# Performance work log

Hardware: AMD Instinct MI355X
Metric: run time of the kernel (lower is better)

Reference implementation:

```python
import jax, jax.numpy as jnp
import numpy as np

H, W, C = 24, 8, 128
HW = H * W  # 192
EPS = 1e-5


def setup_inputs() -> dict:
    key = jax.random.key(0)
    k1, k2 = jax.random.split(key)
    P, G = 64, 64
    prob_fea = jax.random.normal(k1, (P, C, H, W), dtype=jnp.float32)
    gal_fea = jax.random.normal(k2, (G, C, H, W), dtype=jnp.float32)
    bn_gamma = jnp.ones((1,), jnp.float32)
    bn_beta = jnp.zeros((1,), jnp.float32)
    # reset_parameters: fc.weight filled with 1/(H*W)
    fc_w = jnp.full((1, 2 * HW), 1.0 / HW, dtype=jnp.float32)
    fc_b = jnp.zeros((1,), jnp.float32)
    lbn_gamma = jnp.ones((1,), jnp.float32)
    lbn_beta = jnp.zeros((1,), jnp.float32)
    return {"prob_fea": prob_fea, "gal_fea": gal_fea, "bn_gamma": bn_gamma,
            "bn_beta": bn_beta, "fc_w": fc_w, "fc_b": fc_b,
            "lbn_gamma": lbn_gamma, "lbn_beta": lbn_beta}


def reference(prob_fea, gal_fea, bn_gamma, bn_beta, fc_w, fc_b, lbn_gamma, lbn_beta):
    P = prob_fea.shape[0]
    G = gal_fea.shape[0]
    pf = prob_fea.reshape(P, C, HW)  # [P, C, hw]
    gf = gal_fea.reshape(G, C, HW)   # [G, C, hw]
    # all-pairs spatial correlation: score[p, g, r, s] = sum_c pf[p,c,s] * gf[g,c,r]
    score = jnp.einsum('pcs,gcr->pgrs', pf, gf)  # [P, G, hw, hw]
    max_r = jnp.max(score, axis=2)  # max over gallery positions r -> [P, G, hw]
    max_s = jnp.max(score, axis=3)  # max over probe positions s   -> [P, G, hw]
    feat = jnp.concatenate((max_r, max_s), axis=-1).reshape(-1, 2 * HW)  # [P*G, 2hw]
    # BatchNorm1d(1) on [N, 1, 2hw] in training mode: stats over all N*2hw elems
    mu = jnp.mean(feat)
    var = jnp.var(feat)
    feat = (feat - mu) * jax.lax.rsqrt(var + EPS) * bn_gamma[0] + bn_beta[0]
    # fc: [P*G, 2hw] @ [2hw, 1] + b
    logit = feat @ fc_w.T + fc_b  # [P*G, 1]
    # BatchNorm1d(1) on [N, 1]: stats over N
    lmu = jnp.mean(logit)
    lvar = jnp.var(logit)
    logit = (logit - lmu) * jax.lax.rsqrt(lvar + EPS) * lbn_gamma[0] + lbn_beta[0]
    return logit.reshape(P, G)
```

## Files before the change

### kernel.cpp

```cpp
#include <hip/hip_runtime.h>
#include <hip/hip_bf16.h>
#include <stdint.h>

#define HW 192
#define NC 128
#define KEPS 1e-5f
#define QTB 12288

typedef __attribute__((ext_vector_type(8))) short short8;
typedef __attribute__((ext_vector_type(4))) float f32x4;

__device__ __forceinline__ float max3f(float a, float b, float c) {
  float d;
  asm("v_max3_f32 %0, %1, %2, %3" : "=v"(d) : "v"(a), "v"(b), "v"(c));
  return d;
}

__global__ __launch_bounds__(256)
void prep_kernel(const float* __restrict__ prob,
                 const float* __restrict__ gal,
                 unsigned short* __restrict__ probT,
                 unsigned short* __restrict__ galT) {
  __shared__ unsigned short lds[32 * 194];
  const int b = blockIdx.x;
  const int slice = b >> 2;
  const int cc = (b & 3) * 32;
  const bool isProbe = (slice < 64);
  const float* src = isProbe ? prob + (size_t)slice * NC * HW
                             : gal + (size_t)(slice - 64) * NC * HW;
  unsigned short* dst = isProbe ? probT + (size_t)slice * HW * NC
                                : galT + (size_t)(slice - 64) * HW * NC;
  const float* s0 = src + (size_t)cc * HW;
  #pragma unroll
  for (int k = 0; k < 24; ++k) {
    int i = k * 256 + threadIdx.x;
    int cp = i / HW;
    int hw = i - cp * HW;
    lds[cp * 194 + hw] =
        __builtin_bit_cast(unsigned short, __float2bfloat16(s0[i]));
  }
  __syncthreads();
  const int cp = threadIdx.x & 31;
  const int hw0 = threadIdx.x >> 5;
  const int c = cc + cp;
  #pragma unroll
  for (int k = 0; k < 24; ++k) {
    int hw = hw0 + 8 * k;
    unsigned short v = lds[cp * 194 + hw];
    int col = isProbe ? ((((2 * c) ^ ((hw & 7) << 4))) >> 1) : c;
    dst[hw * NC + col] = v;
  }
}

__device__ __forceinline__ void gl_lds16(const void* gsrc, void* ldst) {
  __builtin_amdgcn_global_load_lds(
      (const __attribute__((address_space(1))) void*)gsrc,
      (__attribute__((address_space(3))) void*)ldst, 16, 0, 0);
}

template <int CTRL>
__device__ __forceinline__ float dpp_max(float x) {
  int xi = __builtin_bit_cast(int, x);
  int yi = __builtin_amdgcn_update_dpp(xi, xi, CTRL, 0xf, 0xf, false);
  return fmaxf(x, __builtin_bit_cast(float, yi));
}
__device__ __forceinline__ float ror16_max(float x) {
  x = dpp_max<0x121>(x);
  x = dpp_max<0x122>(x);
  x = dpp_max<0x124>(x);
  x = dpp_max<0x128>(x);
  return x;
}

__global__ __launch_bounds__(256, 3)
void pair_kernel(const unsigned short* __restrict__ galT,
                 const unsigned short* __restrict__ probT,
                 const float* __restrict__ fc_w,
                 float* __restrict__ Wout,
                 float* __restrict__ sPart,
                 float* __restrict__ qPart) {
  __shared__ char ldsP[2][QTB];
  __shared__ float cmP[4][4][192];
  __shared__ float rmF[4][192];
  __shared__ float red[16];
  __shared__ float red2[8];

  const int tid = threadIdx.x;
  const int lane = tid & 63;
  const int wid = tid >> 6;
  const int q = lane >> 4;
  const int r16 = lane & 15;
  const int swz = (r16 & 7) << 4;

  const int g = blockIdx.x >> 4;
  const int pc = blockIdx.x & 15;

  const char* gbase = (const char*)(galT + (size_t)g * HW * NC);
  short8 a[3][4];
  #pragma unroll
  for (int m = 0; m < 3; ++m)
    #pragma unroll
    for (int ks = 0; ks < 4; ++ks)
      a[m][ks] = *(const short8*)(gbase + (wid * 48 + m * 16 + r16) * 256 + ks * 64 + q * 16);

  const float w0 = fc_w[tid];
  const float w1 = (tid < 128) ? fc_w[256 + tid] : 0.f;

  const char* pT = (const char*)probT + (size_t)(pc * 4) * 49152;

  #pragma unroll
  for (int ch = 0; ch < 3; ++ch)
    gl_lds16(pT + ch * 4096 + wid * 1024 + lane * 16,
             &ldsP[0][ch * 4096 + wid * 1024]);

  float rm[3][4];
  const f32x4 zz = (f32x4){0.f, 0.f, 0.f, 0.f};

  for (int t = 0; t < 16; ++t) {
    const int qc = t & 3;
    const int pi = t >> 2;
    __syncthreads();

    if (t + 1 < 16) {
      const char* src = pT + (size_t)(t + 1) * QTB;
      char* dst = ldsP[(t + 1) & 1];
      #pragma unroll
      for (int ch = 0; ch < 3; ++ch)
        gl_lds16(src + ch * 4096 + wid * 1024 + lane * 16,
                 dst + ch * 4096 + wid * 1024);
    }
    const char* cur = ldsP[t & 1];

    __builtin_amdgcn_s_setprio(1);
    f32x4 acc[3][3];
    #pragma unroll
    for (int n = 0; n < 3; ++n) {
      const char* rowB = cur + (n * 16 + r16) * 256;
      #pragma unroll
      for (int ks = 0; ks < 4; ++ks) {
        short8 bf = *(const short8*)(rowB + ((ks * 64 + q * 16) ^ swz));
        #pragma unroll
        for (int m = 0; m < 3; ++m)
          acc[m][n] = __builtin_amdgcn_mfma_f32_16x16x32_bf16(
              a[m][ks], bf, (ks == 0) ? zz : acc[m][n], 0, 0, 0);
      }
    }
    __builtin_amdgcn_s_setprio(0);

    #pragma unroll
    for (int n = 0; n < 3; ++n) {
      float m0 = max3f(acc[0][n][0], acc[0][n][1], acc[0][n][2]);
      float m1 = max3f(acc[0][n][3], acc[1][n][0], acc[1][n][1]);
      float m2 = max3f(acc[1][n][2], acc[1][n][3], acc[2][n][0]);
      float m3 = max3f(acc[2][n][1], acc[2][n][2], acc[2][n][3]);
      float cm = max3f(m0, m1, m2);
      cm = fmaxf(cm, m3);
      cm = fmaxf(cm, __shfl_xor(cm, 16));
      cm = fmaxf(cm, __shfl_xor(cm, 32));
      if (lane < 16) cmP[pi][wid][qc * 48 + n * 16 + r16] = cm;
    }
    #pragma unroll
    for (int m = 0; m < 3; ++m)
      #pragma unroll
      for (int j = 0; j < 4; ++j) {
        float v = max3f(acc[m][0][j], acc[m][1][j], acc[m][2][j]);
        rm[m][j] = (qc == 0) ? v : fmaxf(rm[m][j], v);
      }
    if (qc == 3) {
      #pragma unroll
      for (int m = 0; m < 3; ++m)
        #pragma unroll
        for (int j = 0; j < 4; ++j) {
          float v = ror16_max(rm[m][j]);
          if (r16 == j) rmF[pi][wid * 48 + m * 16 + q * 4 + j] = v;
        }
    }
  }

  __syncthreads();

  float s_acc = 0.f, q_acc = 0.f;
  float wp[4];
  #pragma unroll
  for (int pi = 0; pi < 4; ++pi) {
    float w = 0.f;
    float v0;
    if (tid < 192) {
      float c01 = fmaxf(cmP[pi][0][tid], cmP[pi][1][tid]);
      v0 = max3f(c01, cmP[pi][2][tid], cmP[pi][3][tid]);
    } else {
      v0 = rmF[pi][tid - 192];
    }
    s_acc += v0; q_acc += v0 * v0; w += v0 * w0;
    if (tid < 128) {
      float v1 = rmF[pi][tid + 64];
      s_acc += v1; q_acc += v1 * v1; w += v1 * w1;
    }
    #pragma unroll
    for (int msk = 1; msk < 64; msk <<= 1) w += __shfl_xor(w, msk);
    wp[pi] = w;
  }
  if (lane == 0) {
    #pragma unroll
    for (int pi = 0; pi < 4; ++pi) red[pi * 4 + wid] = wp[pi];
  }
  #pragma unroll
  for (int msk = 1; msk < 64; msk <<= 1) {
    s_acc += __shfl_xor(s_acc, msk);
    q_acc += __shfl_xor(q_acc, msk);
  }
  if (lane == 0) { red2[wid] = s_acc; red2[4 + wid] = q_acc; }
  __syncthreads();
  if (tid < 4)
    Wout[(pc * 4 + tid) * 64 + g] =
        red[tid * 4] + red[tid * 4 + 1] + red[tid * 4 + 2] + red[tid * 4 + 3];
  if (tid == 0) {
    sPart[blockIdx.x] = red2[0] + red2[1] + red2[2] + red2[3];
    qPart[blockIdx.x] = red2[4] + red2[5] + red2[6] + red2[7];
  }
}

__device__ __forceinline__ float block_sum(float v, float* rbuf, float* bc, int nw) {
  int t = threadIdx.x, lane = t & 63, wid = t >> 6;
  #pragma unroll
  for (int m = 1; m < 64; m <<= 1) v += __shfl_xor(v, m);
  if (lane == 0) rbuf[wid] = v;
  __syncthreads();
  if (t == 0) {
    float r = 0.f;
    for (int i = 0; i < nw; ++i) r += rbuf[i];
    bc[0] = r;
  }
  __syncthreads();
  float res = bc[0];
  __syncthreads();
  return res;
}

__global__ __launch_bounds__(1024)
void finalize_kernel(const float* __restrict__ Wv,
                     const float* __restrict__ sPart,
                     const float* __restrict__ qPart,
                     const float* __restrict__ fc_w,
                     const float* __restrict__ fc_b,
                     const float* __restrict__ bn_g,
                     const float* __restrict__ bn_b,
                     const float* __restrict__ lbn_g,
                     const float* __restrict__ lbn_b,
                     float* __restrict__ out) {
  __shared__ float rbuf[16];
  __shared__ float bc[1];
  const int t = threadIdx.x;

  float S = block_sum(sPart[t], rbuf, bc, 16);
  float Q = block_sum(qPart[t], rbuf, bc, 16);
  float SW = block_sum((t < 384) ? fc_w[t] : 0.f, rbuf, bc, 16);

  const float Nf = 4096.0f * 384.0f;
  float mu = S / Nf;
  float var = Q / Nf - mu * mu;
  float istd = rsqrtf(var + KEPS);
  float cA = istd * bn_g[0];
  float off = bn_b[0] * SW + fc_b[0] - cA * mu * SW;

  float l[4];
  float ls = 0.f;
  #pragma unroll
  for (int i = 0; i < 4; ++i) {
    int n = t + i * 1024;
    l[i] = cA * Wv[n] + off;
    ls += l[i];
  }
  float LS = block_sum(ls, rbuf, bc, 16);
  float lmu = LS / 4096.0f;
  float lq = 0.f;
  #pragma unroll
  for (int i = 0; i < 4; ++i) { float d = l[i] - lmu; lq += d * d; }
  float LQ = block_sum(lq, rbuf, bc, 16);
  float lvar = LQ / 4096.0f;
  float sc = lbn_g[0] * rsqrtf(lvar + KEPS);
  float lb = lbn_b[0];
  #pragma unroll
  for (int i = 0; i < 4; ++i) {
    int n = t + i * 1024;
    out[n] = (l[i] - lmu) * sc + lb;
  }
}

extern "C" void kernel_launch(void* const* d_in, const int* in_sizes, int n_in,
                              void* d_out, int out_size, void* d_ws, size_t ws_size,
                              hipStream_t stream) {
  const float* prob  = (const float*)d_in[0];
  const float* gal   = (const float*)d_in[1];
  const float* bn_g  = (const float*)d_in[2];
  const float* bn_b  = (const float*)d_in[3];
  const float* fc_w  = (const float*)d_in[4];
  const float* fc_b  = (const float*)d_in[5];
  const float* lbn_g = (const float*)d_in[6];
  const float* lbn_b = (const float*)d_in[7];
  float* out = (float*)d_out;

  char* ws = (char*)d_ws;
  unsigned short* probT = (unsigned short*)(ws);
  unsigned short* galT  = (unsigned short*)(ws + 3145728);
  float* Wv    = (float*)(ws + 6291456);
  float* sPart = (float*)(ws + 6307840);
  float* qPart = (float*)(ws + 6311936);

  prep_kernel<<<512, 256, 0, stream>>>(prob, gal, probT, galT);
  pair_kernel<<<1024, 256, 0, stream>>>(galT, probT, fc_w, Wv, sPart, qPart);
  finalize_kernel<<<1, 1024, 0, stream>>>(Wv, sPart, qPart, fc_w, fc_b,
                                          bn_g, bn_b, lbn_g, lbn_b, out);
}
```

Measured before the change: 69.96 us.

## Overlap per-probe epilogue with the main loop and double-buffer reduction LDS

The per-probe reduction (column max combine, BN statistics and fc dot product) now runs inside the main loop one probe behind, using parity-indexed cmP/rmF buffers instead of four-slot arrays. This roughly halves the reduction shared memory and allows raising launch bounds from 3 to 4 blocks per SIMD for higher occupancy. The cost is extra work and shuffles inside the loop, reliance on existing barriers for correctness, and tighter register limits that may cause spills given the 12 accumulator tiles and the A fragments kept in registers.

```diff
diff --git a/kernel.cpp b/kernel.cpp
--- a/kernel.cpp
+++ b/kernel.cpp
@@ -72,7 +72,7 @@
   return x;
 }
 
-__global__ __launch_bounds__(256, 3)
+__global__ __launch_bounds__(256, 4)
 void pair_kernel(const unsigned short* __restrict__ galT,
                  const unsigned short* __restrict__ probT,
                  const float* __restrict__ fc_w,
@@ -80,9 +80,9 @@
                  float* __restrict__ sPart,
                  float* __restrict__ qPart) {
   __shared__ char ldsP[2][QTB];
-  __shared__ float cmP[4][4][192];
-  __shared__ float rmF[4][192];
-  __shared__ float red[16];
+  __shared__ float cmP[2][4][192];
+  __shared__ float rmF[2][192];
+  __shared__ float redp[2][4];
   __shared__ float red2[8];
 
   const int tid = threadIdx.x;
@@ -114,11 +114,13 @@
              &ldsP[0][ch * 4096 + wid * 1024]);
 
   float rm[3][4];
+  float s_acc = 0.f, q_acc = 0.f;
   const f32x4 zz = (f32x4){0.f, 0.f, 0.f, 0.f};
 
   for (int t = 0; t < 16; ++t) {
     const int qc = t & 3;
     const int pi = t >> 2;
+    const int par = pi & 1;
     __syncthreads();
 
     if (t + 1 < 16) {
@@ -146,6 +148,34 @@
       }
     }
     __builtin_amdgcn_s_setprio(0);
+
+    if (qc == 0 && t > 0) {
+      const int pp = pi - 1;
+      const int pa = pp & 1;
+      float v;
+      if (tid < 192) {
+        float c01 = fmaxf(cmP[pa][0][tid], cmP[pa][1][tid]);
+        v = max3f(c01, cmP[pa][2][tid], cmP[pa][3][tid]);
+      } else {
+        v = rmF[pa][tid - 192];
+      }
+      s_acc += v; q_acc += v * v;
+      float w = v * w0;
+      if (tid < 128) {
+        float v1 = rmF[pa][tid + 64];
+        s_acc += v1; q_acc += v1 * v1;
+        w += v1 * w1;
+      }
+      #pragma unroll
+      for (int msk = 1; msk < 64; msk <<= 1) w += __shfl_xor(w, msk);
+      if (lane == 0) redp[pa][wid] = w;
+    }
+    if (qc == 1 && t > 1 && tid == 0) {
+      const int pp = pi - 1;
+      const int pa = pp & 1;
+      Wout[(pc * 4 + pp) * 64 + g] =
+          redp[pa][0] + redp[pa][1] + redp[pa][2] + redp[pa][3];
+    }
 
     #pragma unroll
     for (int n = 0; n < 3; ++n) {
@@ -157,7 +187,7 @@
       cm = fmaxf(cm, m3);
       cm = fmaxf(cm, __shfl_xor(cm, 16));
       cm = fmaxf(cm, __shfl_xor(cm, 32));
-      if (lane < 16) cmP[pi][wid][qc * 48 + n * 16 + r16] = cm;
+      if (lane < 16) cmP[par][wid][qc * 48 + n * 16 + r16] = cm;
     }
     #pragma unroll
     for (int m = 0; m < 3; ++m)
@@ -172,37 +202,30 @@
         #pragma unroll
         for (int j = 0; j < 4; ++j) {
           float v = ror16_max(rm[m][j]);
-          if (r16 == j) rmF[pi][wid * 48 + m * 16 + q * 4 + j] = v;
+          if (r16 == j) rmF[par][wid * 48 + m * 16 + q * 4 + j] = v;
         }
     }
   }
 
   __syncthreads();
-
-  float s_acc = 0.f, q_acc = 0.f;
-  float wp[4];
-  #pragma unroll
-  for (int pi = 0; pi < 4; ++pi) {
-    float w = 0.f;
-    float v0;
+  {
+    float v;
     if (tid < 192) {
-      float c01 = fmaxf(cmP[pi][0][tid], cmP[pi][1][tid]);
-      v0 = max3f(c01, cmP[pi][2][tid], cmP[pi][3][tid]);
+      float c01 = fmaxf(cmP[1][0][tid], cmP[1][1][tid]);
+      v = max3f(c01, cmP[1][2][tid], cmP[1][3][tid]);
     } else {
-      v0 = rmF[pi][tid - 192];
-    }
-    s_acc += v0; q_acc += v0 * v0; w += v0 * w0;
+      v = rmF[1][tid - 192];
+    }
+    s_acc += v; q_acc += v * v;
+    float w = v * w0;
     if (tid < 128) {
-      float v1 = rmF[pi][tid + 64];
-      s_acc += v1; q_acc += v1 * v1; w += v1 * w1;
+      float v1 = rmF[1][tid + 64];
+      s_acc += v1; q_acc += v1 * v1;
+      w += v1 * w1;
     }
     #pragma unroll
     for (int msk = 1; msk < 64; msk <<= 1) w += __shfl_xor(w, msk);
-    wp[pi] = w;
-  }
-  if (lane == 0) {
-    #pragma unroll
-    for (int pi = 0; pi < 4; ++pi) red[pi * 4 + wid] = wp[pi];
+    if (lane == 0) redp[1][wid] = w;
   }
   #pragma unroll
   for (int msk = 1; msk < 64; msk <<= 1) {
@@ -211,10 +234,8 @@
   }
   if (lane == 0) { red2[wid] = s_acc; red2[4 + wid] = q_acc; }
   __syncthreads();
-  if (tid < 4)
-    Wout[(pc * 4 + tid) * 64 + g] =
-        red[tid * 4] + red[tid * 4 + 1] + red[tid * 4 + 2] + red[tid * 4 + 3];
   if (tid == 0) {
+    Wout[(pc * 4 + 3) * 64 + g] = redp[1][0] + redp[1][1] + redp[1][2] + redp[1][3];
     sPart[blockIdx.x] = red2[0] + red2[1] + red2[2] + red2[3];
     qPart[blockIdx.x] = red2[4] + red2[5] + red2[6] + red2[7];
   }
```

New measurement: 63.86 us. 1.1x faster.

## Pre-pack operands in MFMA fragment order and load probe tiles directly from global

Applied to the files above, without the earlier changes.

The prep kernel now writes probe and gallery features as bf16 in the exact per-lane MFMA fragment layout, so each lane reads contiguous 16-byte chunks. The pair kernel drops the LDS double-buffered probe staging and its per-step barriers, loading B fragments straight from global or L2. Each block now handles 2 probes instead of 4, so the grid doubles to 2048 blocks and the finalize kernel sums twice as many partials. The change trades LDS traffic and synchronisation for more global/L2 reads, and gallery fragments are reloaded by more blocks.

```diff
diff --git a/kernel.cpp b/kernel.cpp
--- a/kernel.cpp
+++ b/kernel.cpp
@@ -5,7 +5,7 @@
 #define HW 192
 #define NC 128
 #define KEPS 1e-5f
-#define QTB 12288
+#define SLICE_B 49152
 
 typedef __attribute__((ext_vector_type(8))) short short8;
 typedef __attribute__((ext_vector_type(4))) float f32x4;
@@ -19,18 +19,18 @@
 __global__ __launch_bounds__(256)
 void prep_kernel(const float* __restrict__ prob,
                  const float* __restrict__ gal,
-                 unsigned short* __restrict__ probT,
-                 unsigned short* __restrict__ galT) {
+                 char* __restrict__ probF,
+                 char* __restrict__ galF) {
   __shared__ unsigned short lds[32 * 194];
   const int b = blockIdx.x;
   const int slice = b >> 2;
-  const int cc = (b & 3) * 32;
+  const int ks = b & 3;
   const bool isProbe = (slice < 64);
   const float* src = isProbe ? prob + (size_t)slice * NC * HW
                              : gal + (size_t)(slice - 64) * NC * HW;
-  unsigned short* dst = isProbe ? probT + (size_t)slice * HW * NC
-                                : galT + (size_t)(slice - 64) * HW * NC;
-  const float* s0 = src + (size_t)cc * HW;
+  char* dstBase = isProbe ? probF + (size_t)slice * SLICE_B
+                          : galF + (size_t)(slice - 64) * SLICE_B;
+  const float* s0 = src + (size_t)(ks * 32) * HW;
   #pragma unroll
   for (int k = 0; k < 24; ++k) {
     int i = k * 256 + threadIdx.x;
@@ -40,22 +40,22 @@
         __builtin_bit_cast(unsigned short, __float2bfloat16(s0[i]));
   }
   __syncthreads();
-  const int cp = threadIdx.x & 31;
-  const int hw0 = threadIdx.x >> 5;
-  const int c = cc + cp;
-  #pragma unroll
-  for (int k = 0; k < 24; ++k) {
-    int hw = hw0 + 8 * k;
-    unsigned short v = lds[cp * 194 + hw];
-    int col = isProbe ? ((((2 * c) ^ ((hw & 7) << 4))) >> 1) : c;
-    dst[hw * NC + col] = v;
-  }
-}
-
-__device__ __forceinline__ void gl_lds16(const void* gsrc, void* ldst) {
-  __builtin_amdgcn_global_load_lds(
-      (const __attribute__((address_space(1))) void*)gsrc,
-      (__attribute__((address_space(3))) void*)ldst, 16, 0, 0);
+  #pragma unroll
+  for (int rep = 0; rep < 3; ++rep) {
+    int idx = rep * 256 + threadIdx.x;
+    int tile = idx >> 6;
+    int lane = idx & 63;
+    int q = lane >> 4;
+    int r16 = lane & 15;
+    int s = tile * 16 + r16;
+    unsigned short v[8];
+    #pragma unroll
+    for (int j = 0; j < 8; ++j) v[j] = lds[(q * 8 + j) * 194 + s];
+    short8 pack;
+    #pragma unroll
+    for (int j = 0; j < 8; ++j) pack[j] = (short)v[j];
+    *(short8*)(dstBase + (((tile * 4 + ks) * 64 + lane) * 16)) = pack;
+  }
 }
 
 template <int CTRL>
@@ -73,16 +73,15 @@
 }
 
 __global__ __launch_bounds__(256, 3)
-void pair_kernel(const unsigned short* __restrict__ galT,
-                 const unsigned short* __restrict__ probT,
+void pair_kernel(const char* __restrict__ galF,
+                 const char* __restrict__ probF,
                  const float* __restrict__ fc_w,
                  float* __restrict__ Wout,
                  float* __restrict__ sPart,
                  float* __restrict__ qPart) {
-  __shared__ char ldsP[2][QTB];
-  __shared__ float cmP[4][4][192];
-  __shared__ float rmF[4][192];
-  __shared__ float red[16];
+  __shared__ float cmP[2][4][192];
+  __shared__ float rmF[2][192];
+  __shared__ float red[2][4];
   __shared__ float red2[8];
 
   const int tid = threadIdx.x;
@@ -90,119 +89,105 @@
   const int wid = tid >> 6;
   const int q = lane >> 4;
   const int r16 = lane & 15;
-  const int swz = (r16 & 7) << 4;
-
-  const int g = blockIdx.x >> 4;
-  const int pc = blockIdx.x & 15;
-
-  const char* gbase = (const char*)(galT + (size_t)g * HW * NC);
+
+  const int g = blockIdx.x >> 5;
+  const int pc = blockIdx.x & 31;
+
+  const char* gB = galF + (size_t)g * SLICE_B + lane * 16;
   short8 a[3][4];
   #pragma unroll
   for (int m = 0; m < 3; ++m)
     #pragma unroll
     for (int ks = 0; ks < 4; ++ks)
-      a[m][ks] = *(const short8*)(gbase + (wid * 48 + m * 16 + r16) * 256 + ks * 64 + q * 16);
+      a[m][ks] = *(const short8*)(gB + (((wid * 3 + m) * 4 + ks) * 1024));
 
   const float w0 = fc_w[tid];
   const float w1 = (tid < 128) ? fc_w[256 + tid] : 0.f;
 
-  const char* pT = (const char*)probT + (size_t)(pc * 4) * 49152;
-
-  #pragma unroll
-  for (int ch = 0; ch < 3; ++ch)
-    gl_lds16(pT + ch * 4096 + wid * 1024 + lane * 16,
-             &ldsP[0][ch * 4096 + wid * 1024]);
-
-  float rm[3][4];
+  float s_acc = 0.f, q_acc = 0.f;
   const f32x4 zz = (f32x4){0.f, 0.f, 0.f, 0.f};
 
-  for (int t = 0; t < 16; ++t) {
-    const int qc = t & 3;
-    const int pi = t >> 2;
-    __syncthreads();
-
-    if (t + 1 < 16) {
-      const char* src = pT + (size_t)(t + 1) * QTB;
-      char* dst = ldsP[(t + 1) & 1];
-      #pragma unroll
-      for (int ch = 0; ch < 3; ++ch)
-        gl_lds16(src + ch * 4096 + wid * 1024 + lane * 16,
-                 dst + ch * 4096 + wid * 1024);
-    }
-    const char* cur = ldsP[t & 1];
-
-    __builtin_amdgcn_s_setprio(1);
-    f32x4 acc[3][3];
-    #pragma unroll
-    for (int n = 0; n < 3; ++n) {
-      const char* rowB = cur + (n * 16 + r16) * 256;
-      #pragma unroll
-      for (int ks = 0; ks < 4; ++ks) {
-        short8 bf = *(const short8*)(rowB + ((ks * 64 + q * 16) ^ swz));
-        #pragma unroll
-        for (int m = 0; m < 3; ++m)
-          acc[m][n] = __builtin_amdgcn_mfma_f32_16x16x32_bf16(
-              a[m][ks], bf, (ks == 0) ? zz : acc[m][n], 0, 0, 0);
+  #pragma unroll 1
+  for (int pi = 0; pi < 2; ++pi) {
+    const char* pB = probF + (size_t)(pc * 2 + pi) * SLICE_B + lane * 16;
+    float rm[3][4];
+
+    #pragma unroll 1
+    for (int qt = 0; qt < 4; ++qt) {
+      f32x4 acc[3][3];
+      __builtin_amdgcn_s_setprio(1);
+      #pragma unroll
+      for (int nt = 0; nt < 3; ++nt) {
+        const char* bb = pB + ((qt * 3 + nt) * 4) * 1024;
+        short8 b0 = *(const short8*)(bb);
+        short8 b1 = *(const short8*)(bb + 1024);
+        short8 b2 = *(const short8*)(bb + 2048);
+        short8 b3 = *(const short8*)(bb + 3072);
+        #pragma unroll
+        for (int m = 0; m < 3; ++m)
+          acc[m][nt] = __builtin_amdgcn_mfma_f32_16x16x32_bf16(a[m][0], b0, zz, 0, 0, 0);
+        #pragma unroll
+        for (int m = 0; m < 3; ++m)
+          acc[m][nt] = __builtin_amdgcn_mfma_f32_16x16x32_bf16(a[m][1], b1, acc[m][nt], 0, 0, 0);
+        #pragma unroll
+        for (int m = 0; m < 3; ++m)
+          acc[m][nt] = __builtin_amdgcn_mfma_f32_16x16x32_bf16(a[m][2], b2, acc[m][nt], 0, 0, 0);
+        #pragma unroll
+        for (int m = 0; m < 3; ++m)
+          acc[m][nt] = __builtin_amdgcn_mfma_f32_16x16x32_bf16(a[m][3], b3, acc[m][nt], 0, 0, 0);
       }
-    }
-    __builtin_amdgcn_s_setprio(0);
-
-    #pragma unroll
-    for (int n = 0; n < 3; ++n) {
-      float m0 = max3f(acc[0][n][0], acc[0][n][1], acc[0][n][2]);
-      float m1 = max3f(acc[0][n][3], acc[1][n][0], acc[1][n][1]);
-      float m2 = max3f(acc[1][n][2], acc[1][n][3], acc[2][n][0]);
-      float m3 = max3f(acc[2][n][1], acc[2][n][2], acc[2][n][3]);
-      float cm = max3f(m0, m1, m2);
-      cm = fmaxf(cm, m3);
-      cm = fmaxf(cm, __shfl_xor(cm, 16));
-      cm = fmaxf(cm, __shfl_xor(cm, 32));
-      if (lane < 16) cmP[pi][wid][qc * 48 + n * 16 + r16] = cm;
-    }
-    #pragma unroll
-    for (int m = 0; m < 3; ++m)
-      #pragma unroll
-      for (int j = 0; j < 4; ++j) {
-        float v = max3f(acc[m][0][j], acc[m][1][j], acc[m][2][j]);
-        rm[m][j] = (qc == 0) ? v : fmaxf(rm[m][j], v);
+      __builtin_amdgcn_s_setprio(0);
+
+      #pragma unroll
+      for (int nt = 0; nt < 3; ++nt) {
+        float m0 = max3f(acc[0][nt][0], acc[0][nt][1], acc[0][nt][2]);
+        float m1 = max3f(acc[0][nt][3], acc[1][nt][0], acc[1][nt][1]);
+        float m2 = max3f(acc[1][nt][2], acc[1][nt][3], acc[2][nt][0]);
+        float m3 = max3f(acc[2][nt][1], acc[2][nt][2], acc[2][nt][3]);
+        float cm = max3f(m0, m1, m2);
+        cm = fmaxf(cm, m3);
+        cm = fmaxf(cm, __shfl_xor(cm, 16));
+        cm = fmaxf(cm, __shfl_xor(cm, 32));
+        if (lane < 16) cmP[pi][wid][qt * 48 + nt * 16 + r16] = cm;
       }
-    if (qc == 3) {
       #pragma unroll
       for (int m = 0; m < 3; ++m)
         #pragma unroll
         for (int j = 0; j < 4; ++j) {
-          float v = ror16_max(rm[m][j]);
-          if (r16 == j) rmF[pi][wid * 48 + m * 16 + q * 4 + j] = v;
+          float v = max3f(acc[m][0][j], acc[m][1][j], acc[m][2][j]);
+          rm[m][j] = (qt == 0) ? v : fmaxf(rm[m][j], v);
         }
     }
-  }
-
-  __syncthreads();
-
-  float s_acc = 0.f, q_acc = 0.f;
-  float wp[4];
-  #pragma unroll
-  for (int pi = 0; pi < 4; ++pi) {
-    float w = 0.f;
-    float v0;
+    #pragma unroll
+    for (int m = 0; m < 3; ++m)
+      #pragma unroll
+      for (int j = 0; j < 4; ++j) {
+        float v = ror16_max(rm[m][j]);
+        if (r16 == j) rmF[pi][wid * 48 + m * 16 + q * 4 + j] = v;
+      }
+  }
+
+  __syncthreads();
+
+  #pragma unroll
+  for (int pi = 0; pi < 2; ++pi) {
+    float v;
     if (tid < 192) {
       float c01 = fmaxf(cmP[pi][0][tid], cmP[pi][1][tid]);
-      v0 = max3f(c01, cmP[pi][2][tid], cmP[pi][3][tid]);
+      v = max3f(c01, cmP[pi][2][tid], cmP[pi][3][tid]);
     } else {
-      v0 = rmF[pi][tid - 192];
+      v = rmF[pi][tid - 192];
     }
-    s_acc += v0; q_acc += v0 * v0; w += v0 * w0;
+    s_acc += v; q_acc += v * v;
+    float w = v * w0;
     if (tid < 128) {
       float v1 = rmF[pi][tid + 64];
-      s_acc += v1; q_acc += v1 * v1; w += v1 * w1;
+      s_acc += v1; q_acc += v1 * v1;
+      w += v1 * w1;
     }
     #pragma unroll
     for (int msk = 1; msk < 64; msk <<= 1) w += __shfl_xor(w, msk);
-    wp[pi] = w;
-  }
-  if (lane == 0) {
-    #pragma unroll
-    for (int pi = 0; pi < 4; ++pi) red[pi * 4 + wid] = wp[pi];
+    if (lane == 0) red[pi][wid] = w;
   }
   #pragma unroll
   for (int msk = 1; msk < 64; msk <<= 1) {
@@ -211,9 +196,9 @@
   }
   if (lane == 0) { red2[wid] = s_acc; red2[4 + wid] = q_acc; }
   __syncthreads();
-  if (tid < 4)
-    Wout[(pc * 4 + tid) * 64 + g] =
-        red[tid * 4] + red[tid * 4 + 1] + red[tid * 4 + 2] + red[tid * 4 + 3];
+  if (tid < 2)
+    Wout[(pc * 2 + tid) * 64 + g] =
+        red[tid][0] + red[tid][1] + red[tid][2] + red[tid][3];
   if (tid == 0) {
     sPart[blockIdx.x] = red2[0] + red2[1] + red2[2] + red2[3];
     qPart[blockIdx.x] = red2[4] + red2[5] + red2[6] + red2[7];
@@ -252,8 +237,8 @@
   __shared__ float bc[1];
   const int t = threadIdx.x;
 
-  float S = block_sum(sPart[t], rbuf, bc, 16);
-  float Q = block_sum(qPart[t], rbuf, bc, 16);
+  float S = block_sum(sPart[t] + sPart[t + 1024], rbuf, bc, 16);
+  float Q = block_sum(qPart[t] + qPart[t + 1024], rbuf, bc, 16);
   float SW = block_sum((t < 384) ? fc_w[t] : 0.f, rbuf, bc, 16);
 
   const float Nf = 4096.0f * 384.0f;
@@ -301,14 +286,14 @@
   float* out = (float*)d_out;
 
   char* ws = (char*)d_ws;
-  unsigned short* probT = (unsigned short*)(ws);
-  unsigned short* galT  = (unsigned short*)(ws + 3145728);
+  char* probF = ws;
+  char* galF  = ws + 3145728;
   float* Wv    = (float*)(ws + 6291456);
   float* sPart = (float*)(ws + 6307840);
-  float* qPart = (float*)(ws + 6311936);
-
-  prep_kernel<<<512, 256, 0, stream>>>(prob, gal, probT, galT);
-  pair_kernel<<<1024, 256, 0, stream>>>(galT, probT, fc_w, Wv, sPart, qPart);
+  float* qPart = (float*)(ws + 6316032);
+
+  prep_kernel<<<512, 256, 0, stream>>>(prob, gal, probF, galF);
+  pair_kernel<<<2048, 256, 0, stream>>>(galF, probF, fc_w, Wv, sPart, qPart);
   finalize_kernel<<<1, 1024, 0, stream>>>(Wv, sPart, qPart, fc_w, fc_b,
                                           bn_g, bn_b, lbn_g, lbn_b, out);
 }
```

Result: faster. 59.22 us (-15.4%).
